# Kernel optimization log

Measured on AMD Instinct MI355X. Metric: run time of the kernel, lower is better.

The kernel has to match this reference:

```python
import jax, jax.numpy as jnp
import numpy as np

B, L, C, H = 8, 16384, 128, 4
EPS = 1e-5


def setup_inputs() -> dict:
    key = jax.random.key(0)
    k1, k2, k3, k4 = jax.random.split(key, 4)
    return {
        "x": jax.random.normal(k1, (B, L, C), dtype=jnp.float32),
        "W_qkv": jax.random.normal(k2, (3 * C, C), dtype=jnp.float32) * (C ** -0.5),
        "W_out": jax.random.normal(k3, (C, C), dtype=jnp.float32) * (C ** -0.5),
        "b_out": jax.random.normal(k4, (C,), dtype=jnp.float32) * 0.01,
        "gn_w": jnp.ones((C,), dtype=jnp.float32),
        "gn_b": jnp.zeros((C,), dtype=jnp.float32),
    }


def reference(x, W_qkv, W_out, b_out, gn_w, gn_b):
    b, l, c = x.shape
    h = H
    d = c // h                      # dim_head
    scale = d ** -0.5
    xc = jnp.swapaxes(x, 1, 2)      # [b, c, l]
    # 1x1 conv == channel matmul
    qkv = jnp.einsum('oc,bcl->bol', W_qkv, xc)     # [b, 3c, l]
    q, k, v = jnp.split(qkv, 3, axis=1)
    q = q.reshape(b, h, d, l)
    k = k.reshape(b, h, d, l)
    v = v.reshape(b, h, d, l)
    q = jax.nn.softmax(q, axis=2) * scale          # softmax over head-dim
    k = jax.nn.softmax(k, axis=3)                  # softmax over length
    context = jnp.einsum('bhcj,bhdj->bhcd', k, v)  # [b, h, d, d]
    out = jnp.einsum('bhcd,bhdi->bhci', context, q)  # [b, h, d, l]
    out = out.reshape(b, h * d, l)
    out = jnp.einsum('oc,bcl->bol', W_out, out) + b_out[None, :, None]
    # GroupNorm(1, c): normalize over (channel, length) per sample
    mean = jnp.mean(out, axis=(1, 2), keepdims=True)
    var = jnp.var(out, axis=(1, 2), keepdims=True)
    out = (out - mean) * jax.lax.rsqrt(var + EPS)
    out = out * gn_w[None, :, None] + gn_b[None, :, None]
    return jnp.swapaxes(out, 1, 2)                 # [b, l, c]
```

## Files before the change

kernel.cpp:

```cpp
#include <hip/hip_runtime.h>

#define BATCH 8
#define SEQL 16384
#define NCH 128
#define NH 4
#define HD 32
#define GEPS 1e-5f

typedef __bf16 bf16x8 __attribute__((ext_vector_type(8)));
typedef __bf16 bf16x4 __attribute__((ext_vector_type(4)));
typedef float f32x4 __attribute__((ext_vector_type(4)));

#define WKV_B   0
#define WQ_B    65536
#define WO_B    98304
#define CTXB_B  131072
#define CTXF_B  196608
#define ZF_B    327680
#define GNS_B   331776
#define GNF_B   331840
#define ZERO_BYTES (131072 + 4096 + 64 + 64)


__global__ void k_prep(const float* __restrict__ wqkv, const float* __restrict__ wout,
                       char* __restrict__ wsb) {
    int i = blockIdx.x * 256 + threadIdx.x;
    __bf16* wkvb = (__bf16*)(wsb + WKV_B);
    __bf16* wqb  = (__bf16*)(wsb + WQ_B);
    __bf16* wob  = (__bf16*)(wsb + WO_B);
    if (i < 384 * 128) {
        int o = i >> 7, c = i & 127;
        __bf16 v = (__bf16)wqkv[i];
        if (o < 128) wqb[o * 128 + c] = v;
        else         wkvb[(o - 128) * 128 + c] = v;
    }
    if (i < 128 * 128) wob[i] = (__bf16)wout[i];
}

__global__ __launch_bounds__(256, 2) void k_pass1(const float* __restrict__ x,
                                                  char* __restrict__ wsb) {
    __shared__ __attribute__((aligned(16))) __bf16 xb[8352];
    __shared__ __attribute__((aligned(16))) __bf16 ekv[16464];
    const int t = threadIdx.x;
    const int lane = t & 63, wave = t >> 6;
    const int n16 = lane & 15, q = lane >> 4;
    const int batch = blockIdx.x >> 6, sub = blockIdx.x & 63;
    const __bf16* __restrict__ wkvb = (const __bf16*)(wsb + WKV_B);

    bf16x8 aw[4][4];
#pragma unroll
    for (int mt = 0; mt < 4; mt++)
#pragma unroll
        for (int ks = 0; ks < 4; ks++)
            aw[mt][ks] = *(const bf16x8*)&wkvb[(wave * 64 + mt * 16 + n16) * 128 + ks * 32 + q * 8];

    f32x4 ctxacc[2][2];
#pragma unroll
    for (int i = 0; i < 2; i++)
#pragma unroll
        for (int j = 0; j < 2; j++) ctxacc[i][j] = (f32x4){0.f, 0.f, 0.f, 0.f};
    float zacc[4][4];
#pragma unroll
    for (int i = 0; i < 4; i++)
#pragma unroll
        for (int j = 0; j < 4; j++) zacc[i][j] = 0.f;

    for (int rep = 0; rep < 4; rep++) {
        const int chunk = sub + rep * 64;
        const float* xg = x + (size_t)(batch * SEQL + chunk * 64) * NCH;
#pragma unroll
        for (int r = 0; r < 8; r++) {
            int e = t + r * 256;
            int tok = e >> 5, c4 = (e & 31) * 4;
            float4 v = ((const float4*)xg)[e];
            bf16x4 h; h.x = (__bf16)v.x; h.y = (__bf16)v.y; h.z = (__bf16)v.z; h.w = (__bf16)v.w;
            *(bf16x4*)&xb[(c4 >> 5) * 2088 + ((c4 >> 3) & 3) * 520 + tok * 8 + (c4 & 7)] = h;
        }
        __syncthreads();
        f32x4 kvacc[4][4];
#pragma unroll
        for (int i = 0; i < 4; i++)
#pragma unroll
            for (int j = 0; j < 4; j++) kvacc[i][j] = (f32x4){0.f, 0.f, 0.f, 0.f};
#pragma unroll
        for (int ks = 0; ks < 4; ks++) {
            bf16x8 b[4];
#pragma unroll
            for (int nt = 0; nt < 4; nt++)
                b[nt] = *(const bf16x8*)&xb[ks * 2088 + q * 520 + (nt * 16 + n16) * 8];
#pragma unroll
            for (int mt = 0; mt < 4; mt++)
#pragma unroll
                for (int nt = 0; nt < 4; nt++)
                    kvacc[mt][nt] = __builtin_amdgcn_mfma_f32_16x16x32_bf16(
                        aw[mt][ks], b[nt], kvacc[mt][nt], 0, 0, 0);
        }
#pragma unroll
        for (int mt = 0; mt < 4; mt++)
#pragma unroll
            for (int nt = 0; nt < 4; nt++) {
                int tt = nt * 16 + n16;
                int base = (tt >> 5) * 8232 + ((tt >> 3) & 3) * 2056 + (tt & 7);
#pragma unroll
                for (int r = 0; r < 4; r++) {
                    float vv = kvacc[mt][nt][r];
                    if (wave < 2) { vv = __expf(vv); zacc[mt][r] += vv; }
                    int o = wave * 64 + mt * 16 + q * 4 + r;
                    ekv[base + o * 8] = (__bf16)vv;
                }
            }
        __syncthreads();
#pragma unroll
        for (int ks2 = 0; ks2 < 2; ks2++) {
            bf16x8 ea[2], vb[2];
#pragma unroll
            for (int ml = 0; ml < 2; ml++) {
                ea[ml] = *(const bf16x8*)&ekv[ks2 * 8232 + q * 2056 + (wave * 32 + ml * 16 + n16) * 8];
                vb[ml] = *(const bf16x8*)&ekv[ks2 * 8232 + q * 2056 + (128 + wave * 32 + ml * 16 + n16) * 8];
            }
#pragma unroll
            for (int ml = 0; ml < 2; ml++)
#pragma unroll
                for (int nl = 0; nl < 2; nl++)
                    ctxacc[ml][nl] = __builtin_amdgcn_mfma_f32_16x16x32_bf16(
                        ea[ml], vb[nl], ctxacc[ml][nl], 0, 0, 0);
        }
        __syncthreads();
    }
    float* ctxf = (float*)(wsb + CTXF_B) + ((size_t)(batch * 4 + wave) * 32) * 32;
#pragma unroll
    for (int ml = 0; ml < 2; ml++)
#pragma unroll
        for (int nl = 0; nl < 2; nl++)
#pragma unroll
            for (int r = 0; r < 4; r++)
                atomicAdd(&ctxf[(ml * 16 + q * 4 + r) * 32 + nl * 16 + n16], ctxacc[ml][nl][r]);
    if (wave < 2) {
        float* Zf = (float*)(wsb + ZF_B) + batch * 128;
#pragma unroll
        for (int mt = 0; mt < 4; mt++)
#pragma unroll
            for (int r = 0; r < 4; r++) {
                float z = zacc[mt][r];
                z += __shfl_xor(z, 1); z += __shfl_xor(z, 2);
                z += __shfl_xor(z, 4); z += __shfl_xor(z, 8);
                if (n16 == 0) atomicAdd(&Zf[wave * 64 + mt * 16 + q * 4 + r], z);
            }
    }
}

__global__ void k_ctxnorm(char* __restrict__ wsb) {
    int i = blockIdx.x * 256 + threadIdx.x;
    if (i < BATCH * NH * HD * HD) {
        const float* ctxf = (const float*)(wsb + CTXF_B);
        const float* Zf = (const float*)(wsb + ZF_B);
        __bf16* ctxb = (__bf16*)(wsb + CTXB_B);
        int c = (i >> 5) & 31, h = (i >> 10) & 3, b = i >> 12;
        ctxb[i] = (__bf16)(ctxf[i] / Zf[b * 128 + h * 32 + c]);
    }
}

__global__ __launch_bounds__(256, 2) void k_pass2(const float* __restrict__ x,
                                                  const float* __restrict__ bout,
                                                  char* __restrict__ wsb,
                                                  float* __restrict__ out) {
    __shared__ __attribute__((aligned(16))) __bf16 xb[8352];
    __shared__ __attribute__((aligned(16))) __bf16 pB[8352];
    __shared__ __attribute__((aligned(16))) __bf16 attB[8352];
    const int t = threadIdx.x;
    const int lane = t & 63, wave = t >> 6;
    const int n16 = lane & 15, q = lane >> 4;
    const int batch = blockIdx.x >> 6, sub = blockIdx.x & 63;
    const __bf16* __restrict__ wqb = (const __bf16*)(wsb + WQ_B);
    const __bf16* __restrict__ wob = (const __bf16*)(wsb + WO_B);
    const __bf16* __restrict__ ctxb = (const __bf16*)(wsb + CTXB_B);

    bf16x8 aq[2][4], ao[2][4];
#pragma unroll
    for (int ml = 0; ml < 2; ml++)
#pragma unroll
        for (int ks = 0; ks < 4; ks++) {
            aq[ml][ks] = *(const bf16x8*)&wqb[(wave * 32 + ml * 16 + n16) * 128 + ks * 32 + q * 8];
            ao[ml][ks] = *(const bf16x8*)&wob[(wave * 32 + ml * 16 + n16) * 128 + ks * 32 + q * 8];
        }
    bf16x8 actx[2];
#pragma unroll
    for (int ml = 0; ml < 2; ml++)
        actx[ml] = *(const bf16x8*)&ctxb[((size_t)(batch * 4 + wave) * 32 + ml * 16 + n16) * 32 + q * 8];
    float4 bias[2];
#pragma unroll
    for (int ml = 0; ml < 2; ml++)
        bias[ml] = *(const float4*)&bout[wave * 32 + ml * 16 + q * 4];

    float s1 = 0.f, s2 = 0.f;

    for (int rep = 0; rep < 4; rep++) {
        const int chunk = sub + rep * 64;
        const size_t tok0 = (size_t)batch * SEQL + chunk * 64;
        const float* xg = x + tok0 * NCH;
#pragma unroll
        for (int r = 0; r < 8; r++) {
            int e = t + r * 256;
            int tok = e >> 5, c4 = (e & 31) * 4;
            float4 v = ((const float4*)xg)[e];
            bf16x4 h; h.x = (__bf16)v.x; h.y = (__bf16)v.y; h.z = (__bf16)v.z; h.w = (__bf16)v.w;
            *(bf16x4*)&xb[(c4 >> 5) * 2088 + ((c4 >> 3) & 3) * 520 + tok * 8 + (c4 & 7)] = h;
        }
        __syncthreads();
        f32x4 qacc[2][4];
#pragma unroll
        for (int i = 0; i < 2; i++)
#pragma unroll
            for (int j = 0; j < 4; j++) qacc[i][j] = (f32x4){0.f, 0.f, 0.f, 0.f};
#pragma unroll
        for (int ks = 0; ks < 4; ks++) {
            bf16x8 b[4];
#pragma unroll
            for (int nt = 0; nt < 4; nt++)
                b[nt] = *(const bf16x8*)&xb[ks * 2088 + q * 520 + (nt * 16 + n16) * 8];
#pragma unroll
            for (int ml = 0; ml < 2; ml++)
#pragma unroll
                for (int nt = 0; nt < 4; nt++)
                    qacc[ml][nt] = __builtin_amdgcn_mfma_f32_16x16x32_bf16(
                        aq[ml][ks], b[nt], qacc[ml][nt], 0, 0, 0);
        }
#pragma unroll
        for (int nt = 0; nt < 4; nt++) {
            float ss = 0.f;
#pragma unroll
            for (int ml = 0; ml < 2; ml++)
#pragma unroll
                for (int r = 0; r < 4; r++) {
                    float e = __expf(qacc[ml][nt][r]);
                    qacc[ml][nt][r] = e;
                    ss += e;
                }
            ss += __shfl_xor(ss, 16);
            ss += __shfl_xor(ss, 32);
            float inv = 0.17677669529663687f / ss;
#pragma unroll
            for (int ml = 0; ml < 2; ml++)
#pragma unroll
                for (int r = 0; r < 4; r++) qacc[ml][nt][r] *= inv;
        }
#pragma unroll
        for (int ml = 0; ml < 2; ml++)
#pragma unroll
            for (int nt = 0; nt < 4; nt++) {
                bf16x4 h;
                h.x = (__bf16)qacc[ml][nt][0]; h.y = (__bf16)qacc[ml][nt][1];
                h.z = (__bf16)qacc[ml][nt][2]; h.w = (__bf16)qacc[ml][nt][3];
                *(bf16x4*)&pB[wave * 2088 + (ml * 2 + (q >> 1)) * 520 +
                              (nt * 16 + n16) * 8 + (q & 1) * 4] = h;
            }
        __syncthreads();
        f32x4 aacc[2][4];
#pragma unroll
        for (int ml = 0; ml < 2; ml++)
#pragma unroll
            for (int nt = 0; nt < 4; nt++) {
                bf16x8 pb = *(const bf16x8*)&pB[wave * 2088 + q * 520 + (nt * 16 + n16) * 8];
                aacc[ml][nt] = __builtin_amdgcn_mfma_f32_16x16x32_bf16(
                    actx[ml], pb, (f32x4){0.f, 0.f, 0.f, 0.f}, 0, 0, 0);
            }
#pragma unroll
        for (int ml = 0; ml < 2; ml++)
#pragma unroll
            for (int nt = 0; nt < 4; nt++) {
                bf16x4 h;
                h.x = (__bf16)aacc[ml][nt][0]; h.y = (__bf16)aacc[ml][nt][1];
                h.z = (__bf16)aacc[ml][nt][2]; h.w = (__bf16)aacc[ml][nt][3];
                *(bf16x4*)&attB[wave * 2088 + (ml * 2 + (q >> 1)) * 520 +
                                (nt * 16 + n16) * 8 + (q & 1) * 4] = h;
            }
        __syncthreads();
        f32x4 oacc[2][4];
#pragma unroll
        for (int i = 0; i < 2; i++)
#pragma unroll
            for (int j = 0; j < 4; j++) oacc[i][j] = (f32x4){0.f, 0.f, 0.f, 0.f};
#pragma unroll
        for (int ks = 0; ks < 4; ks++) {
            bf16x8 b[4];
#pragma unroll
            for (int nt = 0; nt < 4; nt++)
                b[nt] = *(const bf16x8*)&attB[ks * 2088 + q * 520 + (nt * 16 + n16) * 8];
#pragma unroll
            for (int ml = 0; ml < 2; ml++)
#pragma unroll
                for (int nt = 0; nt < 4; nt++)
                    oacc[ml][nt] = __builtin_amdgcn_mfma_f32_16x16x32_bf16(
                        ao[ml][ks], b[nt], oacc[ml][nt], 0, 0, 0);
        }
#pragma unroll
        for (int ml = 0; ml < 2; ml++)
#pragma unroll
            for (int nt = 0; nt < 4; nt++) {
                float4 vv;
                vv.x = oacc[ml][nt][0] + bias[ml].x;
                vv.y = oacc[ml][nt][1] + bias[ml].y;
                vv.z = oacc[ml][nt][2] + bias[ml].z;
                vv.w = oacc[ml][nt][3] + bias[ml].w;
                s1 += vv.x + vv.y + vv.z + vv.w;
                s2 += vv.x * vv.x + vv.y * vv.y + vv.z * vv.z + vv.w * vv.w;
                *(float4*)&out[(tok0 + nt * 16 + n16) * NCH + wave * 32 + ml * 16 + q * 4] = vv;
            }
        __syncthreads();
    }
#pragma unroll
    for (int off = 32; off > 0; off >>= 1) {
        s1 += __shfl_xor(s1, off);
        s2 += __shfl_xor(s2, off);
    }
    if (lane == 0) {
        float* gns = (float*)(wsb + GNS_B);
        atomicAdd(&gns[batch * 2 + 0], s1);
        atomicAdd(&gns[batch * 2 + 1], s2);
    }
}

__global__ void k_gnfinal(char* __restrict__ wsb) {
    int b = threadIdx.x;
    if (b < BATCH) {
        const float n = (float)NCH * (float)SEQL;
        const float* gns = (const float*)(wsb + GNS_B);
        float* gnf = (float*)(wsb + GNF_B);
        float mean = gns[b * 2] / n;
        float var = gns[b * 2 + 1] / n - mean * mean;
        gnf[b * 2] = mean;
        gnf[b * 2 + 1] = rsqrtf(var + GEPS);
    }
}

__global__ __launch_bounds__(256) void k_gnorm(float* __restrict__ out,
                                               const char* __restrict__ wsb,
                                               const float* __restrict__ gw,
                                               const float* __restrict__ gb) {
    size_t i4 = (size_t)blockIdx.x * 256 + threadIdx.x;
    int b = (int)(i4 >> 19);
    int c4 = (int)(i4 & 31);
    const float* gnf = (const float*)(wsb + GNF_B);
    float mean = gnf[b * 2], rstd = gnf[b * 2 + 1];
    float4 w = *(const float4*)&gw[c4 * 4];
    float4 bb = *(const float4*)&gb[c4 * 4];
    float4 v = ((float4*)out)[i4];
    v.x = (v.x - mean) * rstd * w.x + bb.x;
    v.y = (v.y - mean) * rstd * w.y + bb.y;
    v.z = (v.z - mean) * rstd * w.z + bb.z;
    v.w = (v.w - mean) * rstd * w.w + bb.w;
    ((float4*)out)[i4] = v;
}

extern "C" void kernel_launch(void* const* d_in, const int* in_sizes, int n_in,
                              void* d_out, int out_size, void* d_ws, size_t ws_size,
                              hipStream_t stream) {
    const float* x    = (const float*)d_in[0];
    const float* wqkv = (const float*)d_in[1];
    const float* wout = (const float*)d_in[2];
    const float* bout = (const float*)d_in[3];
    const float* gw   = (const float*)d_in[4];
    const float* gb   = (const float*)d_in[5];
    float* out = (float*)d_out;
    char* wsb  = (char*)d_ws;

    hipMemsetAsync(wsb + CTXF_B, 0, ZERO_BYTES, stream);
    k_prep<<<192, 256, 0, stream>>>(wqkv, wout, wsb);
    k_pass1<<<512, 256, 0, stream>>>(x, wsb);
    k_ctxnorm<<<128, 256, 0, stream>>>(wsb);
    k_pass2<<<512, 256, 0, stream>>>(x, bout, wsb, out);
    k_gnfinal<<<1, 64, 0, stream>>>(wsb);
    k_gnorm<<<16384, 256, 0, stream>>>(out, wsb, gw, gb);
}
```

Before: 229.2 us.

## Use one block per 64-token chunk in both attention passes for higher occupancy

Both pass kernels drop the 4-iteration per-block chunk loop and instead launch four times as many blocks, each handling a single 64-token chunk. Weight fragments are reloaded per k-step instead of being held in registers, pass1 computes kv in two halves to shrink accumulators, and pass2 reuses the x buffer for the attention output to cut LDS. Launch bounds rise to 3 and 4 blocks per CU to raise occupancy and latency hiding. The cost is 4x more context atomics in pass1 and repeated weight loads per block; pass2 reduces its GroupNorm partials in shared memory first, so it issues one atomic pair per block.

```diff
diff --git a/kernel.cpp b/kernel.cpp
--- a/kernel.cpp
+++ b/kernel.cpp
@@ -37,96 +37,95 @@
     if (i < 128 * 128) wob[i] = (__bf16)wout[i];
 }
 
-__global__ __launch_bounds__(256, 2) void k_pass1(const float* __restrict__ x,
+__global__ __launch_bounds__(256, 3) void k_pass1(const float* __restrict__ x,
                                                   char* __restrict__ wsb) {
     __shared__ __attribute__((aligned(16))) __bf16 xb[8352];
     __shared__ __attribute__((aligned(16))) __bf16 ekv[16464];
     const int t = threadIdx.x;
     const int lane = t & 63, wave = t >> 6;
     const int n16 = lane & 15, q = lane >> 4;
-    const int batch = blockIdx.x >> 6, sub = blockIdx.x & 63;
+    const int batch = blockIdx.x >> 8, chunk = blockIdx.x & 255;
     const __bf16* __restrict__ wkvb = (const __bf16*)(wsb + WKV_B);
 
-    bf16x8 aw[4][4];
-#pragma unroll
-    for (int mt = 0; mt < 4; mt++)
-#pragma unroll
-        for (int ks = 0; ks < 4; ks++)
-            aw[mt][ks] = *(const bf16x8*)&wkvb[(wave * 64 + mt * 16 + n16) * 128 + ks * 32 + q * 8];
-
-    f32x4 ctxacc[2][2];
-#pragma unroll
-    for (int i = 0; i < 2; i++)
-#pragma unroll
-        for (int j = 0; j < 2; j++) ctxacc[i][j] = (f32x4){0.f, 0.f, 0.f, 0.f};
+    const float* xg = x + (size_t)(batch * SEQL + chunk * 64) * NCH;
+#pragma unroll
+    for (int r = 0; r < 8; r++) {
+        int e = t + r * 256;
+        int tok = e >> 5, c4 = (e & 31) * 4;
+        float4 v = ((const float4*)xg)[e];
+        bf16x4 h; h.x = (__bf16)v.x; h.y = (__bf16)v.y; h.z = (__bf16)v.z; h.w = (__bf16)v.w;
+        *(bf16x4*)&xb[(c4 >> 5) * 2088 + ((c4 >> 3) & 3) * 520 + tok * 8 + (c4 & 7)] = h;
+    }
+    __syncthreads();
+
     float zacc[4][4];
 #pragma unroll
     for (int i = 0; i < 4; i++)
 #pragma unroll
         for (int j = 0; j < 4; j++) zacc[i][j] = 0.f;
 
-    for (int rep = 0; rep < 4; rep++) {
-        const int chunk = sub + rep * 64;
-        const float* xg = x + (size_t)(batch * SEQL + chunk * 64) * NCH;
-#pragma unroll
-        for (int r = 0; r < 8; r++) {
-            int e = t + r * 256;
-            int tok = e >> 5, c4 = (e & 31) * 4;
-            float4 v = ((const float4*)xg)[e];
-            bf16x4 h; h.x = (__bf16)v.x; h.y = (__bf16)v.y; h.z = (__bf16)v.z; h.w = (__bf16)v.w;
-            *(bf16x4*)&xb[(c4 >> 5) * 2088 + ((c4 >> 3) & 3) * 520 + tok * 8 + (c4 & 7)] = h;
-        }
-        __syncthreads();
-        f32x4 kvacc[4][4];
+#pragma unroll
+    for (int half = 0; half < 2; half++) {
+        f32x4 kvacc[4][2];
 #pragma unroll
         for (int i = 0; i < 4; i++)
 #pragma unroll
-            for (int j = 0; j < 4; j++) kvacc[i][j] = (f32x4){0.f, 0.f, 0.f, 0.f};
+            for (int j = 0; j < 2; j++) kvacc[i][j] = (f32x4){0.f, 0.f, 0.f, 0.f};
 #pragma unroll
         for (int ks = 0; ks < 4; ks++) {
-            bf16x8 b[4];
-#pragma unroll
-            for (int nt = 0; nt < 4; nt++)
-                b[nt] = *(const bf16x8*)&xb[ks * 2088 + q * 520 + (nt * 16 + n16) * 8];
+            bf16x8 aw_k[4];
 #pragma unroll
             for (int mt = 0; mt < 4; mt++)
-#pragma unroll
-                for (int nt = 0; nt < 4; nt++)
-                    kvacc[mt][nt] = __builtin_amdgcn_mfma_f32_16x16x32_bf16(
-                        aw[mt][ks], b[nt], kvacc[mt][nt], 0, 0, 0);
+                aw_k[mt] = *(const bf16x8*)&wkvb[(wave * 64 + mt * 16 + n16) * 128 + ks * 32 + q * 8];
+            bf16x8 b[2];
+#pragma unroll
+            for (int nl = 0; nl < 2; nl++)
+                b[nl] = *(const bf16x8*)&xb[ks * 2088 + q * 520 + ((half * 2 + nl) * 16 + n16) * 8];
+#pragma unroll
+            for (int mt = 0; mt < 4; mt++)
+#pragma unroll
+                for (int nl = 0; nl < 2; nl++)
+                    kvacc[mt][nl] = __builtin_amdgcn_mfma_f32_16x16x32_bf16(
+                        aw_k[mt], b[nl], kvacc[mt][nl], 0, 0, 0);
         }
 #pragma unroll
         for (int mt = 0; mt < 4; mt++)
 #pragma unroll
-            for (int nt = 0; nt < 4; nt++) {
-                int tt = nt * 16 + n16;
+            for (int nl = 0; nl < 2; nl++) {
+                int tt = (half * 2 + nl) * 16 + n16;
                 int base = (tt >> 5) * 8232 + ((tt >> 3) & 3) * 2056 + (tt & 7);
 #pragma unroll
                 for (int r = 0; r < 4; r++) {
-                    float vv = kvacc[mt][nt][r];
+                    float vv = kvacc[mt][nl][r];
                     if (wave < 2) { vv = __expf(vv); zacc[mt][r] += vv; }
                     int o = wave * 64 + mt * 16 + q * 4 + r;
                     ekv[base + o * 8] = (__bf16)vv;
                 }
             }
-        __syncthreads();
-#pragma unroll
-        for (int ks2 = 0; ks2 < 2; ks2++) {
-            bf16x8 ea[2], vb[2];
-#pragma unroll
-            for (int ml = 0; ml < 2; ml++) {
-                ea[ml] = *(const bf16x8*)&ekv[ks2 * 8232 + q * 2056 + (wave * 32 + ml * 16 + n16) * 8];
-                vb[ml] = *(const bf16x8*)&ekv[ks2 * 8232 + q * 2056 + (128 + wave * 32 + ml * 16 + n16) * 8];
-            }
-#pragma unroll
-            for (int ml = 0; ml < 2; ml++)
-#pragma unroll
-                for (int nl = 0; nl < 2; nl++)
-                    ctxacc[ml][nl] = __builtin_amdgcn_mfma_f32_16x16x32_bf16(
-                        ea[ml], vb[nl], ctxacc[ml][nl], 0, 0, 0);
-        }
-        __syncthreads();
-    }
+    }
+    __syncthreads();
+
+    f32x4 ctxacc[2][2];
+#pragma unroll
+    for (int i = 0; i < 2; i++)
+#pragma unroll
+        for (int j = 0; j < 2; j++) ctxacc[i][j] = (f32x4){0.f, 0.f, 0.f, 0.f};
+#pragma unroll
+    for (int ks2 = 0; ks2 < 2; ks2++) {
+        bf16x8 ea[2], vb[2];
+#pragma unroll
+        for (int ml = 0; ml < 2; ml++) {
+            ea[ml] = *(const bf16x8*)&ekv[ks2 * 8232 + q * 2056 + (wave * 32 + ml * 16 + n16) * 8];
+            vb[ml] = *(const bf16x8*)&ekv[ks2 * 8232 + q * 2056 + (128 + wave * 32 + ml * 16 + n16) * 8];
+        }
+#pragma unroll
+        for (int ml = 0; ml < 2; ml++)
+#pragma unroll
+            for (int nl = 0; nl < 2; nl++)
+                ctxacc[ml][nl] = __builtin_amdgcn_mfma_f32_16x16x32_bf16(
+                    ea[ml], vb[nl], ctxacc[ml][nl], 0, 0, 0);
+    }
+
     float* ctxf = (float*)(wsb + CTXF_B) + ((size_t)(batch * 4 + wave) * 32) * 32;
 #pragma unroll
     for (int ml = 0; ml < 2; ml++)
@@ -160,163 +159,160 @@
     }
 }
 
-__global__ __launch_bounds__(256, 2) void k_pass2(const float* __restrict__ x,
+__global__ __launch_bounds__(256, 4) void k_pass2(const float* __restrict__ x,
                                                   const float* __restrict__ bout,
                                                   char* __restrict__ wsb,
                                                   float* __restrict__ out) {
     __shared__ __attribute__((aligned(16))) __bf16 xb[8352];
     __shared__ __attribute__((aligned(16))) __bf16 pB[8352];
-    __shared__ __attribute__((aligned(16))) __bf16 attB[8352];
+    __shared__ float gred[8];
     const int t = threadIdx.x;
     const int lane = t & 63, wave = t >> 6;
     const int n16 = lane & 15, q = lane >> 4;
-    const int batch = blockIdx.x >> 6, sub = blockIdx.x & 63;
+    const int batch = blockIdx.x >> 8, chunk = blockIdx.x & 255;
     const __bf16* __restrict__ wqb = (const __bf16*)(wsb + WQ_B);
     const __bf16* __restrict__ wob = (const __bf16*)(wsb + WO_B);
     const __bf16* __restrict__ ctxb = (const __bf16*)(wsb + CTXB_B);
 
-    bf16x8 aq[2][4], ao[2][4];
-#pragma unroll
-    for (int ml = 0; ml < 2; ml++)
-#pragma unroll
-        for (int ks = 0; ks < 4; ks++) {
-            aq[ml][ks] = *(const bf16x8*)&wqb[(wave * 32 + ml * 16 + n16) * 128 + ks * 32 + q * 8];
-            ao[ml][ks] = *(const bf16x8*)&wob[(wave * 32 + ml * 16 + n16) * 128 + ks * 32 + q * 8];
-        }
+    const size_t tok0 = (size_t)batch * SEQL + chunk * 64;
+    const float* xg = x + tok0 * NCH;
+#pragma unroll
+    for (int r = 0; r < 8; r++) {
+        int e = t + r * 256;
+        int tok = e >> 5, c4 = (e & 31) * 4;
+        float4 v = ((const float4*)xg)[e];
+        bf16x4 h; h.x = (__bf16)v.x; h.y = (__bf16)v.y; h.z = (__bf16)v.z; h.w = (__bf16)v.w;
+        *(bf16x4*)&xb[(c4 >> 5) * 2088 + ((c4 >> 3) & 3) * 520 + tok * 8 + (c4 & 7)] = h;
+    }
+    __syncthreads();
+
+    f32x4 qacc[2][4];
+#pragma unroll
+    for (int i = 0; i < 2; i++)
+#pragma unroll
+        for (int j = 0; j < 4; j++) qacc[i][j] = (f32x4){0.f, 0.f, 0.f, 0.f};
+#pragma unroll
+    for (int ks = 0; ks < 4; ks++) {
+        bf16x8 aq_k[2];
+#pragma unroll
+        for (int ml = 0; ml < 2; ml++)
+            aq_k[ml] = *(const bf16x8*)&wqb[(wave * 32 + ml * 16 + n16) * 128 + ks * 32 + q * 8];
+        bf16x8 b[4];
+#pragma unroll
+        for (int nt = 0; nt < 4; nt++)
+            b[nt] = *(const bf16x8*)&xb[ks * 2088 + q * 520 + (nt * 16 + n16) * 8];
+#pragma unroll
+        for (int ml = 0; ml < 2; ml++)
+#pragma unroll
+            for (int nt = 0; nt < 4; nt++)
+                qacc[ml][nt] = __builtin_amdgcn_mfma_f32_16x16x32_bf16(
+                    aq_k[ml], b[nt], qacc[ml][nt], 0, 0, 0);
+    }
+#pragma unroll
+    for (int nt = 0; nt < 4; nt++) {
+        float ss = 0.f;
+#pragma unroll
+        for (int ml = 0; ml < 2; ml++)
+#pragma unroll
+            for (int r = 0; r < 4; r++) {
+                float e = __expf(qacc[ml][nt][r]);
+                qacc[ml][nt][r] = e;
+                ss += e;
+            }
+        ss += __shfl_xor(ss, 16);
+        ss += __shfl_xor(ss, 32);
+        float inv = 0.17677669529663687f / ss;
+#pragma unroll
+        for (int ml = 0; ml < 2; ml++)
+#pragma unroll
+            for (int r = 0; r < 4; r++) qacc[ml][nt][r] *= inv;
+    }
+#pragma unroll
+    for (int ml = 0; ml < 2; ml++)
+#pragma unroll
+        for (int nt = 0; nt < 4; nt++) {
+            bf16x4 h;
+            h.x = (__bf16)qacc[ml][nt][0]; h.y = (__bf16)qacc[ml][nt][1];
+            h.z = (__bf16)qacc[ml][nt][2]; h.w = (__bf16)qacc[ml][nt][3];
+            *(bf16x4*)&pB[wave * 2088 + (ml * 2 + (q >> 1)) * 520 +
+                          (nt * 16 + n16) * 8 + (q & 1) * 4] = h;
+        }
+    __syncthreads();
     bf16x8 actx[2];
 #pragma unroll
     for (int ml = 0; ml < 2; ml++)
         actx[ml] = *(const bf16x8*)&ctxb[((size_t)(batch * 4 + wave) * 32 + ml * 16 + n16) * 32 + q * 8];
+    f32x4 aacc[2][4];
+#pragma unroll
+    for (int ml = 0; ml < 2; ml++)
+#pragma unroll
+        for (int nt = 0; nt < 4; nt++) {
+            bf16x8 pb = *(const bf16x8*)&pB[wave * 2088 + q * 520 + (nt * 16 + n16) * 8];
+            aacc[ml][nt] = __builtin_amdgcn_mfma_f32_16x16x32_bf16(
+                actx[ml], pb, (f32x4){0.f, 0.f, 0.f, 0.f}, 0, 0, 0);
+        }
+    __bf16* attB = xb;
+#pragma unroll
+    for (int ml = 0; ml < 2; ml++)
+#pragma unroll
+        for (int nt = 0; nt < 4; nt++) {
+            bf16x4 h;
+            h.x = (__bf16)aacc[ml][nt][0]; h.y = (__bf16)aacc[ml][nt][1];
+            h.z = (__bf16)aacc[ml][nt][2]; h.w = (__bf16)aacc[ml][nt][3];
+            *(bf16x4*)&attB[wave * 2088 + (ml * 2 + (q >> 1)) * 520 +
+                            (nt * 16 + n16) * 8 + (q & 1) * 4] = h;
+        }
+    __syncthreads();
+    f32x4 oacc[2][4];
+#pragma unroll
+    for (int i = 0; i < 2; i++)
+#pragma unroll
+        for (int j = 0; j < 4; j++) oacc[i][j] = (f32x4){0.f, 0.f, 0.f, 0.f};
+#pragma unroll
+    for (int ks = 0; ks < 4; ks++) {
+        bf16x8 ao_k[2];
+#pragma unroll
+        for (int ml = 0; ml < 2; ml++)
+            ao_k[ml] = *(const bf16x8*)&wob[(wave * 32 + ml * 16 + n16) * 128 + ks * 32 + q * 8];
+        bf16x8 b[4];
+#pragma unroll
+        for (int nt = 0; nt < 4; nt++)
+            b[nt] = *(const bf16x8*)&attB[ks * 2088 + q * 520 + (nt * 16 + n16) * 8];
+#pragma unroll
+        for (int ml = 0; ml < 2; ml++)
+#pragma unroll
+            for (int nt = 0; nt < 4; nt++)
+                oacc[ml][nt] = __builtin_amdgcn_mfma_f32_16x16x32_bf16(
+                    ao_k[ml], b[nt], oacc[ml][nt], 0, 0, 0);
+    }
     float4 bias[2];
 #pragma unroll
     for (int ml = 0; ml < 2; ml++)
         bias[ml] = *(const float4*)&bout[wave * 32 + ml * 16 + q * 4];
-
     float s1 = 0.f, s2 = 0.f;
-
-    for (int rep = 0; rep < 4; rep++) {
-        const int chunk = sub + rep * 64;
-        const size_t tok0 = (size_t)batch * SEQL + chunk * 64;
-        const float* xg = x + tok0 * NCH;
-#pragma unroll
-        for (int r = 0; r < 8; r++) {
-            int e = t + r * 256;
-            int tok = e >> 5, c4 = (e & 31) * 4;
-            float4 v = ((const float4*)xg)[e];
-            bf16x4 h; h.x = (__bf16)v.x; h.y = (__bf16)v.y; h.z = (__bf16)v.z; h.w = (__bf16)v.w;
-            *(bf16x4*)&xb[(c4 >> 5) * 2088 + ((c4 >> 3) & 3) * 520 + tok * 8 + (c4 & 7)] = h;
-        }
-        __syncthreads();
-        f32x4 qacc[2][4];
-#pragma unroll
-        for (int i = 0; i < 2; i++)
-#pragma unroll
-            for (int j = 0; j < 4; j++) qacc[i][j] = (f32x4){0.f, 0.f, 0.f, 0.f};
-#pragma unroll
-        for (int ks = 0; ks < 4; ks++) {
-            bf16x8 b[4];
-#pragma unroll
-            for (int nt = 0; nt < 4; nt++)
-                b[nt] = *(const bf16x8*)&xb[ks * 2088 + q * 520 + (nt * 16 + n16) * 8];
-#pragma unroll
-            for (int ml = 0; ml < 2; ml++)
-#pragma unroll
-                for (int nt = 0; nt < 4; nt++)
-                    qacc[ml][nt] = __builtin_amdgcn_mfma_f32_16x16x32_bf16(
-                        aq[ml][ks], b[nt], qacc[ml][nt], 0, 0, 0);
-        }
+#pragma unroll
+    for (int ml = 0; ml < 2; ml++)
 #pragma unroll
         for (int nt = 0; nt < 4; nt++) {
-            float ss = 0.f;
-#pragma unroll
-            for (int ml = 0; ml < 2; ml++)
-#pragma unroll
-                for (int r = 0; r < 4; r++) {
-                    float e = __expf(qacc[ml][nt][r]);
-                    qacc[ml][nt][r] = e;
-                    ss += e;
-                }
-            ss += __shfl_xor(ss, 16);
-            ss += __shfl_xor(ss, 32);
-            float inv = 0.17677669529663687f / ss;
-#pragma unroll
-            for (int ml = 0; ml < 2; ml++)
-#pragma unroll
-                for (int r = 0; r < 4; r++) qacc[ml][nt][r] *= inv;
-        }
-#pragma unroll
-        for (int ml = 0; ml < 2; ml++)
-#pragma unroll
-            for (int nt = 0; nt < 4; nt++) {
-                bf16x4 h;
-                h.x = (__bf16)qacc[ml][nt][0]; h.y = (__bf16)qacc[ml][nt][1];
-                h.z = (__bf16)qacc[ml][nt][2]; h.w = (__bf16)qacc[ml][nt][3];
-                *(bf16x4*)&pB[wave * 2088 + (ml * 2 + (q >> 1)) * 520 +
-                              (nt * 16 + n16) * 8 + (q & 1) * 4] = h;
-            }
-        __syncthreads();
-        f32x4 aacc[2][4];
-#pragma unroll
-        for (int ml = 0; ml < 2; ml++)
-#pragma unroll
-            for (int nt = 0; nt < 4; nt++) {
-                bf16x8 pb = *(const bf16x8*)&pB[wave * 2088 + q * 520 + (nt * 16 + n16) * 8];
-                aacc[ml][nt] = __builtin_amdgcn_mfma_f32_16x16x32_bf16(
-                    actx[ml], pb, (f32x4){0.f, 0.f, 0.f, 0.f}, 0, 0, 0);
-            }
-#pragma unroll
-        for (int ml = 0; ml < 2; ml++)
-#pragma unroll
-            for (int nt = 0; nt < 4; nt++) {
-                bf16x4 h;
-                h.x = (__bf16)aacc[ml][nt][0]; h.y = (__bf16)aacc[ml][nt][1];
-                h.z = (__bf16)aacc[ml][nt][2]; h.w = (__bf16)aacc[ml][nt][3];
-                *(bf16x4*)&attB[wave * 2088 + (ml * 2 + (q >> 1)) * 520 +
-                                (nt * 16 + n16) * 8 + (q & 1) * 4] = h;
-            }
-        __syncthreads();
-        f32x4 oacc[2][4];
-#pragma unroll
-        for (int i = 0; i < 2; i++)
-#pragma unroll
-            for (int j = 0; j < 4; j++) oacc[i][j] = (f32x4){0.f, 0.f, 0.f, 0.f};
-#pragma unroll
-        for (int ks = 0; ks < 4; ks++) {
-            bf16x8 b[4];
-#pragma unroll
-            for (int nt = 0; nt < 4; nt++)
-                b[nt] = *(const bf16x8*)&attB[ks * 2088 + q * 520 + (nt * 16 + n16) * 8];
-#pragma unroll
-            for (int ml = 0; ml < 2; ml++)
-#pragma unroll
-                for (int nt = 0; nt < 4; nt++)
-                    oacc[ml][nt] = __builtin_amdgcn_mfma_f32_16x16x32_bf16(
-                        ao[ml][ks], b[nt], oacc[ml][nt], 0, 0, 0);
-        }
-#pragma unroll
-        for (int ml = 0; ml < 2; ml++)
-#pragma unroll
-            for (int nt = 0; nt < 4; nt++) {
-                float4 vv;
-                vv.x = oacc[ml][nt][0] + bias[ml].x;
-                vv.y = oacc[ml][nt][1] + bias[ml].y;
-                vv.z = oacc[ml][nt][2] + bias[ml].z;
-                vv.w = oacc[ml][nt][3] + bias[ml].w;
-                s1 += vv.x + vv.y + vv.z + vv.w;
-                s2 += vv.x * vv.x + vv.y * vv.y + vv.z * vv.z + vv.w * vv.w;
-                *(float4*)&out[(tok0 + nt * 16 + n16) * NCH + wave * 32 + ml * 16 + q * 4] = vv;
-            }
-        __syncthreads();
-    }
+            float4 vv;
+            vv.x = oacc[ml][nt][0] + bias[ml].x;
+            vv.y = oacc[ml][nt][1] + bias[ml].y;
+            vv.z = oacc[ml][nt][2] + bias[ml].z;
+            vv.w = oacc[ml][nt][3] + bias[ml].w;
+            s1 += vv.x + vv.y + vv.z + vv.w;
+            s2 += vv.x * vv.x + vv.y * vv.y + vv.z * vv.z + vv.w * vv.w;
+            *(float4*)&out[(tok0 + nt * 16 + n16) * NCH + wave * 32 + ml * 16 + q * 4] = vv;
+        }
 #pragma unroll
     for (int off = 32; off > 0; off >>= 1) {
         s1 += __shfl_xor(s1, off);
         s2 += __shfl_xor(s2, off);
     }
-    if (lane == 0) {
-        float* gns = (float*)(wsb + GNS_B);
-        atomicAdd(&gns[batch * 2 + 0], s1);
-        atomicAdd(&gns[batch * 2 + 1], s2);
+    if (lane == 0) { gred[wave * 2 + 0] = s1; gred[wave * 2 + 1] = s2; }
+    __syncthreads();
+    if (t < 2) {
+        float s = gred[t] + gred[2 + t] + gred[4 + t] + gred[6 + t];
+        atomicAdd(&((float*)(wsb + GNS_B))[batch * 2 + t], s);
     }
 }
 
@@ -366,9 +362,9 @@
 
     hipMemsetAsync(wsb + CTXF_B, 0, ZERO_BYTES, stream);
     k_prep<<<192, 256, 0, stream>>>(wqkv, wout, wsb);
-    k_pass1<<<512, 256, 0, stream>>>(x, wsb);
+    k_pass1<<<2048, 256, 0, stream>>>(x, wsb);
     k_ctxnorm<<<128, 256, 0, stream>>>(wsb);
-    k_pass2<<<512, 256, 0, stream>>>(x, bout, wsb, out);
+    k_pass2<<<2048, 256, 0, stream>>>(x, bout, wsb, out);
     k_gnfinal<<<1, 64, 0, stream>>>(wsb);
     k_gnorm<<<16384, 256, 0, stream>>>(out, wsb, gw, gb);
 }
```

Result: slower. 281.9 us (+23.0%).
